# Kernel optimization log

Measured on AMD Instinct MI355X. Metric: run time of the kernel, lower is better.

## Reference

```python
import jax, jax.numpy as jnp
import numpy as np

B, S, DIM = 1, 2048, 1024
HEADS, KV_HEADS, DH = 16, 2, 64
GQ = HEADS // KV_HEADS
CBS = 64   # compress block size
SBS = 64   # selection block size
NUM_SEL = 8
WIN = 512  # sliding window size
NUM_MEM = 1
SCALE = DH ** -0.5
NEG = -jnp.finfo(jnp.float32).max


def setup_inputs():
    ks = jax.random.split(jax.random.key(0), 12)
    cdim = CBS * DH
    dim_inner = HEADS * DH
    dim_kv = KV_HEADS * DH
    p = lambda k, shape: jax.random.normal(k, shape, jnp.float32) * 0.02
    return {
        "x": jax.random.normal(ks[0], (B, S, DIM), jnp.float32),
        "rms_g": jnp.ones((DIM,), jnp.float32),
        "W_qkv": p(ks[1], (DIM, dim_inner + 2 * dim_kv)),
        "k_pos": p(ks[2], (KV_HEADS, CBS, DH)),
        "v_pos": p(ks[3], (KV_HEADS, CBS, DH)),
        "mem_kv": p(ks[4], (2, KV_HEADS, NUM_MEM, DH)),
        "kW1": p(ks[5], (cdim, cdim)), "kb1": jnp.zeros((cdim,), jnp.float32),
        "kW2": p(ks[6], (cdim, DH)), "kb2": jnp.zeros((DH,), jnp.float32),
        "vW1": p(ks[7], (cdim, cdim)), "vb1": jnp.zeros((cdim,), jnp.float32),
        "vW2": p(ks[8], (cdim, DH)), "vb2": jnp.zeros((DH,), jnp.float32),
        "W_comb": p(ks[9], (DIM, 3 * HEADS)),
        "b_comb": jnp.tile(jnp.array([-2.0, -2.0, 2.0], jnp.float32), HEADS),
        "W_out": p(ks[10], (HEADS * DH, DIM)),
    }


def _rot_half(u):
    v = u.reshape(u.shape[:-1] + (DH // 2, 2))
    return jnp.stack([-v[..., 1], v[..., 0]], axis=-1).reshape(u.shape)


def reference(x, rms_g, W_qkv, k_pos, v_pos, mem_kv, kW1, kb1, kW2, kb2,
              vW1, vb1, vW2, vb2, W_comb, b_comb, W_out):
    n_cb = S // CBS
    n_fb = S // SBS
    num_sel = min(NUM_SEL, n_cb)

    # RMSNorm
    xn = x * jax.lax.rsqrt(jnp.mean(x * x, -1, keepdims=True) + jnp.finfo(jnp.float32).eps) * rms_g

    qkv = xn @ W_qkv
    q, k, v = jnp.split(qkv, [HEADS * DH, (HEADS + KV_HEADS) * DH], axis=-1)
    q = q.reshape(B, S, HEADS, DH).transpose(0, 2, 1, 3)       # b h n d
    k = k.reshape(B, S, KV_HEADS, DH).transpose(0, 2, 1, 3)
    v = v.reshape(B, S, KV_HEADS, DH).transpose(0, 2, 1, 3)

    # ---- compressed branch: per-block MLP compression of K/V ----
    kc = (k + jnp.tile(k_pos, (1, n_cb, 1))[None]).reshape(B, KV_HEADS, n_cb, CBS * DH)
    vc = (v + jnp.tile(v_pos, (1, n_cb, 1))[None]).reshape(B, KV_HEADS, n_cb, CBS * DH)
    ck = jax.nn.relu(kc @ kW1 + kb1) @ kW2 + kb2               # b h w d
    cv = jax.nn.relu(vc @ vW1 + vb1) @ vW2 + vb2
    ck = jnp.concatenate([jnp.broadcast_to(mem_kv[0], (B, KV_HEADS, NUM_MEM, DH)), ck], axis=2)
    cv = jnp.concatenate([jnp.broadcast_to(mem_kv[1], (B, KV_HEADS, NUM_MEM, DH)), cv], axis=2)
    ck_seq = jnp.concatenate([jnp.full((NUM_MEM,), -1), (jnp.arange(n_cb) + 1) * CBS - 1])
    cmask = ck_seq[None, :] < jnp.arange(S)[:, None]           # [S, mem+n_cb]
    qg = q.reshape(B, KV_HEADS, GQ, S, DH)
    csim = jnp.einsum('bhgid,bhjd->bhgij', qg, ck) * SCALE
    csim = jnp.where(cmask, csim, NEG)
    c_out = jnp.einsum('bhgij,bhjd->bhgid', jax.nn.softmax(csim, -1), cv).reshape(B, HEADS, S, DH)

    # ---- rotary embedding (interleaved pairs, theta=10000) ----
    inv_freq = 1.0 / (10000.0 ** (jnp.arange(0, DH, 2, dtype=jnp.float32) / DH))
    freqs = jnp.repeat(jnp.arange(S, dtype=jnp.float32)[:, None] * inv_freq, 2, axis=-1)
    cos, sin = jnp.cos(freqs), jnp.sin(freqs)
    rq = q * cos + _rot_half(q) * sin
    rk = k * cos + _rot_half(k) * sin

    # ---- block selection from compressed attention scores ----
    imp = csim[..., NUM_MEM:].mean(axis=2)                     # mean over grouped queries: [B,KVH,S,n_cb]
    imp = jnp.concatenate([jnp.full(imp.shape[:-1] + (1,), -1000.0), imp], -1)
    imp = jax.nn.softmax(imp, -1)[..., 1:]
    sel_val, sel_idx = jax.lax.top_k(imp, num_sel)             # [B,KVH,S,sel]
    fmask = jnp.broadcast_to((sel_val > 1e-10)[..., None], (B, KV_HEADS, S, num_sel, SBS))
    diag_idx = jnp.broadcast_to((jnp.arange(S) // SBS)[None, None, :, None], (B, KV_HEADS, S, 1))
    sel_idx = jnp.concatenate([sel_idx, diag_idx], -1)         # append own (diagonal) block
    causal = jnp.tril(jnp.ones((SBS, SBS), bool))
    diag_mask = jnp.broadcast_to(jnp.tile(causal, (n_fb, 1))[None, None, :, None, :], (B, KV_HEADS, S, 1, SBS))
    fmask = jnp.concatenate([fmask, diag_mask], axis=-2).reshape(B, KV_HEADS, S, (num_sel + 1) * SBS)

    # ---- fine attention over gathered selected blocks ----
    fkb = rk.reshape(B, KV_HEADS, 1, n_fb, SBS, DH)
    fvb = v.reshape(B, KV_HEADS, 1, n_fb, SBS, DH)
    gi = sel_idx[..., None, None]                              # [B,KVH,S,sel+1,1,1]
    fk = jnp.take_along_axis(fkb, gi, axis=3).reshape(B, KV_HEADS, S, (num_sel + 1) * SBS, DH)
    fv = jnp.take_along_axis(fvb, gi, axis=3).reshape(B, KV_HEADS, S, (num_sel + 1) * SBS, DH)
    fqg = rq.reshape(B, KV_HEADS, GQ, S, DH)
    fsim = jnp.einsum('bhgid,bhijd->bhgij', fqg, fk) * SCALE
    fsim = jnp.where(fmask[:, :, None], fsim, NEG)
    f_out = jnp.einsum('bhgij,bhijd->bhgid', jax.nn.softmax(fsim, -1), fv).reshape(B, HEADS, S, DH)

    # ---- causal sliding window (exact window, look_backward=1) ----
    skf = jnp.repeat(rk, GQ, axis=1)
    svf = jnp.repeat(v, GQ, axis=1)
    nw = S // WIN
    kw = skf.reshape(B, HEADS, nw, WIN, DH)
    vw = svf.reshape(B, HEADS, nw, WIN, DH)
    kcat = jnp.concatenate([jnp.pad(kw, ((0, 0), (0, 0), (1, 0), (0, 0), (0, 0)))[:, :, :nw], kw], axis=3)
    vcat = jnp.concatenate([jnp.pad(vw, ((0, 0), (0, 0), (1, 0), (0, 0), (0, 0)))[:, :, :nw], vw], axis=3)
    qw = rq.reshape(B, HEADS, nw, WIN, DH)
    gq_pos = jnp.arange(nw)[:, None, None] * WIN + jnp.arange(WIN)[None, :, None]
    gk_pos = jnp.arange(nw)[:, None, None] * WIN - WIN + jnp.arange(2 * WIN)[None, None, :]
    smask = (gk_pos >= 0) & (gk_pos <= gq_pos) & (gq_pos - gk_pos <= WIN)
    ssim = jnp.where(smask, jnp.einsum('bhwid,bhwjd->bhwij', qw, kcat) * SCALE, NEG)
    s_out = jnp.einsum('bhwij,bhwjd->bhwid', jax.nn.softmax(ssim, -1), vcat).reshape(B, HEADS, S, DH)

    # ---- learned per-token, per-head strategy combination ----
    gates = jax.nn.sigmoid(xn @ W_comb + b_comb).reshape(B, S, HEADS, 3).transpose(0, 2, 1, 3)
    out = gates[..., 0:1] * c_out + gates[..., 1:2] * f_out + gates[..., 2:3] * s_out
    return out.transpose(0, 2, 1, 3).reshape(B, S, HEADS * DH) @ W_out
```

## Files before the change

kernel.cpp:

```cpp
#include <hip/hip_runtime.h>
#include <hip/hip_bf16.h>
#include <cstddef>
#include <cstdint>

#define S      2048
#define DIM    1024
#define HEADS  16
#define KVH    2
#define GQ     8
#define DH     64
#define CBS    64
#define SBS    64
#define NUMSEL 8
#define WIN    512
#define NCB    (S / CBS)
#define CDIM   (CBS * DH)
#define QKVC   (HEADS * DH + 2 * KVH * DH)
#define KOFF   (HEADS * DH)
#define VOFF   (HEADS * DH + KVH * DH)
#define SCALE  0.125f
#define RMS_EPS 1.1920928955078125e-07f

typedef __attribute__((ext_vector_type(8))) short bf16x8;
typedef __attribute__((ext_vector_type(4))) float f32x4;

__device__ inline short f2bs(float f) {
    __hip_bfloat16 b = __float2bfloat16(f);
    return *(short*)&b;
}

__device__ inline float wave_sum(float v) {
    for (int o = 32; o > 0; o >>= 1) v += __shfl_xor(v, o);
    return v;
}

__global__ __launch_bounds__(256) void rmsnorm_kernel(
        const float* __restrict__ x, const float* __restrict__ g,
        float* __restrict__ xn, __hip_bfloat16* __restrict__ xnb) {
    int s = blockIdx.x, tid = threadIdx.x;
    const float4* row = (const float4*)(x + (size_t)s * DIM);
    float4 v = row[tid];
    float ss = v.x * v.x + v.y * v.y + v.z * v.z + v.w * v.w;
    ss = wave_sum(ss);
    __shared__ float red[4];
    if ((tid & 63) == 0) red[tid >> 6] = ss;
    __syncthreads();
    float tot = red[0] + red[1] + red[2] + red[3];
    float sc = rsqrtf(tot / (float)DIM + RMS_EPS);
    float4 gg = ((const float4*)g)[tid];
    float4 o;
    o.x = v.x * sc * gg.x; o.y = v.y * sc * gg.y;
    o.z = v.z * sc * gg.z; o.w = v.w * sc * gg.w;
    ((float4*)(xn + (size_t)s * DIM))[tid] = o;
    size_t b = (size_t)s * DIM + tid * 4;
    xnb[b + 0] = __float2bfloat16(o.x);
    xnb[b + 1] = __float2bfloat16(o.y);
    xnb[b + 2] = __float2bfloat16(o.z);
    xnb[b + 3] = __float2bfloat16(o.w);
}

__global__ __launch_bounds__(256) void cast_bf16_kernel(
        const float* __restrict__ in, __hip_bfloat16* __restrict__ out, int n4) {
    int e = blockIdx.x * 256 + threadIdx.x;
    if (e >= n4) return;
    float4 v = ((const float4*)in)[e];
    out[4 * e + 0] = __float2bfloat16(v.x);
    out[4 * e + 1] = __float2bfloat16(v.y);
    out[4 * e + 2] = __float2bfloat16(v.z);
    out[4 * e + 3] = __float2bfloat16(v.w);
}

__global__ __launch_bounds__(256) void transpose_cast_kernel(
        const float* __restrict__ W, short* __restrict__ Wt, int K, int N) {
    __shared__ float tile[64][65];
    int n0 = blockIdx.x * 64, k0 = blockIdx.y * 64;
    int tid = threadIdx.x;
    #pragma unroll
    for (int e = 0; e < 16; e++) {
        int idx = tid + e * 256;
        int r = idx >> 6, c = idx & 63;
        float v = 0.f;
        if (n0 + c < N) v = W[(size_t)(k0 + r) * N + n0 + c];
        tile[r][c] = v;
    }
    __syncthreads();
    #pragma unroll
    for (int e = 0; e < 16; e++) {
        int idx = tid + e * 256;
        int r = idx >> 6, c = idx & 63;
        if (n0 + r < N)
            Wt[(size_t)(n0 + r) * K + k0 + c] = f2bs(tile[c][r]);
    }
}

__global__ __launch_bounds__(256) void cast_v_kernel(
        const float* __restrict__ qkv, short* __restrict__ vb) {
    int e = blockIdx.x * 256 + threadIdx.x;
    if (e >= S * KVH * DH / 4) return;
    int idx = e * 4;
    int tok = idx / (KVH * DH), rem = idx % (KVH * DH);
    float4 v = *(const float4*)(qkv + (size_t)tok * QKVC + VOFF + rem);
    vb[idx + 0] = f2bs(v.x);
    vb[idx + 1] = f2bs(v.y);
    vb[idx + 2] = f2bs(v.z);
    vb[idx + 3] = f2bs(v.w);
}

template <int BM, int BN, int WM, int WN, int ACT>
__global__ __launch_bounds__(256) void gemm_bt_kernel(
        const __hip_bfloat16* __restrict__ A, const short* __restrict__ Bt,
        const float* __restrict__ bias, float* __restrict__ C,
        int M, int N, int K) {
    constexpr int BK = 32;
    constexpr int TM = BM / (WM * 16);
    constexpr int TN = BN / (WN * 16);
    constexpr int LDK = BK + 8;
    __shared__ short As[BM][LDK];
    __shared__ short Bs[BN][LDK];
    int tid = threadIdx.x;
    int wave = tid >> 6, lane = tid & 63;
    int wm = wave % WM, wn = wave / WM;
    int m0 = wm * TM * 16, n0 = wn * TN * 16;
    int bm = blockIdx.y * BM, bn = blockIdx.x * BN;
    int lm = lane & 15, quad = lane >> 4;
    const short* Ash = (const short*)A;
    f32x4 acc[TM][TN] = {};
    for (int k0 = 0; k0 < K; k0 += BK) {
        #pragma unroll
        for (int e = 0; e < BM * BK / (256 * 8); e++) {
            int idx = (tid + e * 256) * 8;
            int r = idx >> 5, kk = idx & 31;
            *(bf16x8*)(&As[r][kk]) =
                *(const bf16x8*)(Ash + (size_t)(bm + r) * K + k0 + kk);
        }
        #pragma unroll
        for (int e = 0; e < BN * BK / (256 * 8); e++) {
            int idx = (tid + e * 256) * 8;
            int r = idx >> 5, kk = idx & 31;
            bf16x8 v = {};
            if (bn + r < N)
                v = *(const bf16x8*)(Bt + (size_t)(bn + r) * K + k0 + kk);
            *(bf16x8*)(&Bs[r][kk]) = v;
        }
        __syncthreads();
        bf16x8 af[TM], bf_[TN];
        #pragma unroll
        for (int i = 0; i < TM; i++)
            af[i] = *(const bf16x8*)(&As[m0 + i * 16 + lm][quad * 8]);
        #pragma unroll
        for (int j = 0; j < TN; j++)
            bf_[j] = *(const bf16x8*)(&Bs[n0 + j * 16 + lm][quad * 8]);
        #pragma unroll
        for (int i = 0; i < TM; i++)
            #pragma unroll
            for (int j = 0; j < TN; j++)
                acc[i][j] = __builtin_amdgcn_mfma_f32_16x16x32_bf16(
                    af[i], bf_[j], acc[i][j], 0, 0, 0);
        __syncthreads();
    }
    #pragma unroll
    for (int i = 0; i < TM; i++) {
        #pragma unroll
        for (int j = 0; j < TN; j++) {
            int gn = bn + n0 + j * 16 + lm;
            if (gn >= N) continue;
            #pragma unroll
            for (int r = 0; r < 4; r++) {
                int gm = bm + m0 + i * 16 + quad * 4 + r;
                float v = acc[i][j][r];
                if (bias) v += bias[gn];
                if (ACT == 2) v = 1.f / (1.f + expf(-v));
                C[(size_t)gm * N + gn] = v;
            }
        }
    }
}

template <int BM, int BN, int WM, int WN>
__global__ __launch_bounds__(256) void gemm_mfma_kernel(
        const __hip_bfloat16* __restrict__ A, const float* __restrict__ B,
        float* __restrict__ C, int M, int N, int K, int kslice) {
    constexpr int BK = 32;
    constexpr int TM = BM / (WM * 16);
    constexpr int TN = BN / (WN * 16);
    constexpr int LDK = BK + 8;
    constexpr int NB = BN * BK / 256;
    __shared__ __hip_bfloat16 As[BM][LDK];
    __shared__ __hip_bfloat16 Bs[BN][LDK];
    int tid = threadIdx.x;
    int wave = tid >> 6, lane = tid & 63;
    int wm = wave % WM, wn = wave / WM;
    int m0 = wm * TM * 16, n0 = wn * TN * 16;
    int bm = blockIdx.y * BM, bn = blockIdx.x * BN;
    int kbeg = blockIdx.z * kslice, kend = kbeg + kslice;
    int lm = lane & 15, quad = lane >> 4;
    f32x4 acc[TM][TN] = {};
    for (int k0 = kbeg; k0 < kend; k0 += BK) {
        #pragma unroll
        for (int e = 0; e < BM * BK / (256 * 8); e++) {
            int idx = (tid + e * 256) * 8;
            int r = idx >> 5, kk = idx & 31;
            *(bf16x8*)(&As[r][kk]) =
                *(const bf16x8*)(A + (size_t)(bm + r) * K + k0 + kk);
        }
        float tmpB[NB];
        #pragma unroll
        for (int e = 0; e < NB; e++) {
            int idx = tid + e * 256;
            int kk = idx / BN, n = idx % BN;
            tmpB[e] = B[(size_t)(k0 + kk) * N + bn + n];
        }
        #pragma unroll
        for (int e = 0; e < NB; e++) {
            int idx = tid + e * 256;
            int kk = idx / BN, n = idx % BN;
            Bs[n][kk] = __float2bfloat16(tmpB[e]);
        }
        __syncthreads();
        bf16x8 af[TM], bf_[TN];
        #pragma unroll
        for (int i = 0; i < TM; i++)
            af[i] = *(const bf16x8*)(&As[m0 + i * 16 + lm][quad * 8]);
        #pragma unroll
        for (int j = 0; j < TN; j++)
            bf_[j] = *(const bf16x8*)(&Bs[n0 + j * 16 + lm][quad * 8]);
        #pragma unroll
        for (int i = 0; i < TM; i++)
            #pragma unroll
            for (int j = 0; j < TN; j++)
                acc[i][j] = __builtin_amdgcn_mfma_f32_16x16x32_bf16(
                    af[i], bf_[j], acc[i][j], 0, 0, 0);
        __syncthreads();
    }
    size_t cbase = (size_t)blockIdx.z * M * N;
    #pragma unroll
    for (int i = 0; i < TM; i++) {
        #pragma unroll
        for (int j = 0; j < TN; j++) {
            int gn = bn + n0 + j * 16 + lm;
            #pragma unroll
            for (int r = 0; r < 4; r++) {
                int gm = bm + m0 + i * 16 + quad * 4 + r;
                C[cbase + (size_t)gm * N + gn] = acc[i][j][r];
            }
        }
    }
}

__global__ __launch_bounds__(256) void gemm_splitk_kernel(
        const float* __restrict__ A, const float* __restrict__ B,
        float* __restrict__ P, int M, int N, int K, int kslice) {
    const int BM = 64, BN = 64, BK = 16;
    __shared__ float As[BK][BM + 4];
    __shared__ float Bs[BK][BN];
    int bm = blockIdx.y * BM, bn = blockIdx.x * BN;
    int z = blockIdx.z;
    int kbeg = z * kslice, kend = kbeg + kslice;
    int tid = threadIdx.x;
    int tx = tid & 15, ty = tid >> 4;
    float acc[4][4] = {{0.f}};
    for (int k0 = kbeg; k0 < kend; k0 += BK) {
        #pragma unroll
        for (int e = 0; e < 4; e++) {
            int idx = tid + e * 256;
            int m = idx >> 4, kk = idx & 15;
            int gm = bm + m;
            As[kk][m] = (gm < M) ? A[(size_t)gm * K + k0 + kk] : 0.f;
        }
        #pragma unroll
        for (int e = 0; e < 4; e++) {
            int idx = tid + e * 256;
            int kk = idx >> 6, n = idx & 63;
            int gn = bn + n;
            Bs[kk][n] = (gn < N) ? B[(size_t)(k0 + kk) * N + gn] : 0.f;
        }
        __syncthreads();
        #pragma unroll
        for (int kk = 0; kk < BK; kk++) {
            float a[4], b[4];
            #pragma unroll
            for (int i = 0; i < 4; i++) a[i] = As[kk][ty * 4 + i];
            #pragma unroll
            for (int j = 0; j < 4; j++) b[j] = Bs[kk][tx * 4 + j];
            #pragma unroll
            for (int i = 0; i < 4; i++)
                #pragma unroll
                for (int j = 0; j < 4; j++) acc[i][j] += a[i] * b[j];
        }
        __syncthreads();
    }
    #pragma unroll
    for (int i = 0; i < 4; i++) {
        int gm = bm + ty * 4 + i;
        if (gm >= M) continue;
        #pragma unroll
        for (int j = 0; j < 4; j++) {
            int gn = bn + tx * 4 + j;
            if (gn >= N) continue;
            P[((size_t)z * M + gm) * N + gn] = acc[i][j];
        }
    }
}

template <int ACT>
__global__ __launch_bounds__(256) void reduce_splitk_kernel(
        const float* __restrict__ P, const float* __restrict__ bias,
        float* __restrict__ C, int MN, int N, int splits) {
    int e = blockIdx.x * 256 + threadIdx.x;
    if (e >= MN) return;
    float s = 0.f;
    for (int z = 0; z < splits; z++) s += P[(size_t)z * MN + e];
    s += bias[e % N];
    if (ACT == 1) s = fmaxf(s, 0.f);
    C[e] = s;
}

__global__ __launch_bounds__(256) void rotary_kernel(
        const float* __restrict__ qkv, short* __restrict__ rqb, short* __restrict__ rkb) {
    int s = blockIdx.x, tid = threadIdx.x;
    for (int p = tid; p < (HEADS + KVH) * (DH / 2); p += 256) {
        int t; const float* src; short* dst;
        if (p < HEADS * (DH / 2)) {
            int h = p >> 5; t = p & 31;
            src = qkv + (size_t)s * QKVC + h * DH + 2 * t;
            dst = rqb + (size_t)s * (HEADS * DH) + h * DH + 2 * t;
        } else {
            int pp = p - HEADS * (DH / 2);
            int h = pp >> 5; t = pp & 31;
            src = qkv + (size_t)s * QKVC + KOFF + h * DH + 2 * t;
            dst = rkb + (size_t)s * (KVH * DH) + h * DH + 2 * t;
        }
        float u0 = src[0], u1 = src[1];
        float freq = powf(10000.f, -((float)(2 * t) / (float)DH));
        float ang = (float)s * freq;
        float sn, cs;
        sincosf(ang, &sn, &cs);
        dst[0] = f2bs(u0 * cs - u1 * sn);
        dst[1] = f2bs(u1 * cs + u0 * sn);
    }
}

__global__ __launch_bounds__(256) void build_cmat_kernel(
        const float* __restrict__ qkv, const float* __restrict__ k_pos,
        const float* __restrict__ v_pos, __hip_bfloat16* __restrict__ kcm,
        __hip_bfloat16* __restrict__ vcm) {
    int r = blockIdx.x;
    int h = r >> 5, w = r & 31;
    for (int e = threadIdx.x; e < CDIM; e += 256) {
        int i = e >> 6, d = e & 63;
        size_t qb = (size_t)(w * CBS + i) * QKVC;
        kcm[(size_t)r * CDIM + e] =
            __float2bfloat16(qkv[qb + KOFF + h * DH + d] + k_pos[(h * CBS + i) * DH + d]);
        vcm[(size_t)r * CDIM + e] =
            __float2bfloat16(qkv[qb + VOFF + h * DH + d] + v_pos[(h * CBS + i) * DH + d]);
    }
}

__global__ __launch_bounds__(256) void assemble_kernel(
        const float* __restrict__ ckb, const float* __restrict__ cvb,
        const float* __restrict__ mem_kv, float* __restrict__ ck, float* __restrict__ cv,
        short* __restrict__ ck16, short* __restrict__ cv16) {
    int e = blockIdx.x * 256 + threadIdx.x;
    if (e >= KVH * (NCB + 1) * DH) return;
    int d = e & 63;
    int j = (e >> 6) % (NCB + 1);
    int h = e / ((NCB + 1) * DH);
    float kv, vv;
    if (j == 0) {
        kv = mem_kv[0 * KVH * DH + h * DH + d];
        vv = mem_kv[1 * KVH * DH + h * DH + d];
    } else {
        kv = ckb[((size_t)h * NCB + j - 1) * DH + d];
        vv = cvb[((size_t)h * NCB + j - 1) * DH + d];
    }
    ck[e] = kv; cv[e] = vv;
    ck16[e] = f2bs(kv); cv16[e] = f2bs(vv);
}

__global__ __launch_bounds__(64) void imp_kernel(
        const float* __restrict__ qkv, const float* __restrict__ ck,
        float* __restrict__ imp) {
    int kvh = blockIdx.x, s = blockIdx.y, t = threadIdx.x;
    __shared__ float qg[GQ * DH];
    __shared__ float ckl[NCB * 65];
    for (int e = t; e < GQ * DH; e += 64) {
        int g = e >> 6, d = e & 63;
        qg[e] = qkv[(size_t)s * QKVC + (kvh * GQ + g) * DH + d];
    }
    for (int e = t; e < NCB * DH; e += 64) {
        int w = e >> 6, d = e & 63;
        ckl[w * 65 + d] = ck[((size_t)kvh * (NCB + 1) + 1 + w) * DH + d];
    }
    __syncthreads();
    if (t < NCB) {
        int w = t;
        float val;
        if (w * CBS + CBS - 1 < s) {
            float acc = 0.f;
            #pragma unroll
            for (int g = 0; g < GQ; g++) {
                const float* qp = qg + g * DH;
                const float* cp = ckl + w * 65;
                #pragma unroll 16
                for (int d = 0; d < DH; d++) acc += qp[d] * cp[d];
            }
            val = acc * SCALE * (1.f / (float)GQ);
        } else {
            val = -INFINITY;
        }
        imp[((size_t)kvh * S + s) * NCB + w] = val;
    }
}

__global__ __launch_bounds__(256) void select_kernel(
        const float* __restrict__ imp, int* __restrict__ sel) {
    int idx = blockIdx.x * 256 + threadIdx.x;
    if (idx >= KVH * S) return;
    const float* row = imp + (size_t)idx * NCB;
    float p[NCB];
    float m = -1000.f;
    for (int w = 0; w < NCB; w++) { p[w] = row[w]; m = fmaxf(m, p[w]); }
    float z = expf(-1000.f - m);
    for (int w = 0; w < NCB; w++) { p[w] = expf(p[w] - m); z += p[w]; }
    float inv = 1.f / z;
    bool used[NCB];
    for (int w = 0; w < NCB; w++) used[w] = false;
    for (int i = 0; i < NUMSEL; i++) {
        int best = 0; float bv = -1.f;
        for (int w = 0; w < NCB; w++) {
            if (!used[w]) {
                float pw = p[w] * inv;
                if (pw > bv) { bv = pw; best = w; }
            }
        }
        used[best] = true;
        sel[(size_t)idx * NUMSEL + i] = (bv > 1e-10f) ? best : -1;
    }
}

__global__ __launch_bounds__(256) void cattn_kernel(
        const float* __restrict__ qkv, const short* __restrict__ ck16,
        const short* __restrict__ cv16, const float* __restrict__ gates,
        float* __restrict__ attn) {
    int h = blockIdx.x, qb = blockIdx.y;
    int kvh = h >> 3;
    int tid = threadIdx.x;
    int wv = tid >> 6, lane = tid & 63;
    int lm = lane & 15, quad = lane >> 4;
    __shared__ short Qb[64][72];
    __shared__ short Ks[64][72];
    __shared__ short Vt[64][72];
    __shared__ short Pb[64][72];
    for (int e = tid; e < 1024; e += 256) {
        int q = e >> 4, d4 = (e & 15) * 4;
        float4 v = *(const float4*)(qkv + (size_t)(qb * 64 + q) * QKVC + h * DH + d4);
        Qb[q][d4 + 0] = f2bs(v.x); Qb[q][d4 + 1] = f2bs(v.y);
        Qb[q][d4 + 2] = f2bs(v.z); Qb[q][d4 + 3] = f2bs(v.w);
    }
    for (int e = tid; e < 512; e += 256) {
        int c8 = e >> 6, j = e & 63;
        bf16x8 kv = {}, vv = {};
        if (j < NCB + 1) {
            kv = *(const bf16x8*)(ck16 + ((size_t)kvh * (NCB + 1) + j) * DH + c8 * 8);
            vv = *(const bf16x8*)(cv16 + ((size_t)kvh * (NCB + 1) + j) * DH + c8 * 8);
        }
        #pragma unroll
        for (int t = 0; t < 8; t++) {
            Ks[j][c8 * 8 + t] = kv[t];
            Vt[c8 * 8 + t][j] = vv[t];
        }
    }
    __syncthreads();
    bf16x8 aq0 = *(const bf16x8*)&Qb[wv * 16 + lm][quad * 8];
    bf16x8 aq1 = *(const bf16x8*)&Qb[wv * 16 + lm][32 + quad * 8];
    int vismax = (qb < NCB) ? qb : NCB;
    f32x4 sc[4];
    #pragma unroll
    for (int t = 0; t < 4; t++) {
        bf16x8 bk0 = *(const bf16x8*)&Ks[t * 16 + lm][quad * 8];
        bf16x8 bk1 = *(const bf16x8*)&Ks[t * 16 + lm][32 + quad * 8];
        f32x4 s4 = {0.f, 0.f, 0.f, 0.f};
        s4 = __builtin_amdgcn_mfma_f32_16x16x32_bf16(aq0, bk0, s4, 0, 0, 0);
        s4 = __builtin_amdgcn_mfma_f32_16x16x32_bf16(aq1, bk1, s4, 0, 0, 0);
        sc[t] = s4;
    }
    float l[4];
    float pr[4][4];
    #pragma unroll
    for (int r = 0; r < 4; r++) {
        float mx = -INFINITY;
        #pragma unroll
        for (int t = 0; t < 4; t++) {
            int jj = t * 16 + lm;
            bool vis = (jj == 0) || (jj <= vismax);
            float v = vis ? sc[t][r] * SCALE : -INFINITY;
            sc[t][r] = v;
            mx = fmaxf(mx, v);
        }
        #pragma unroll
        for (int o = 1; o < 16; o <<= 1) mx = fmaxf(mx, __shfl_xor(mx, o));
        float sum = 0.f;
        #pragma unroll
        for (int t = 0; t < 4; t++) {
            float p = expf(sc[t][r] - mx);
            pr[r][t] = p;
            sum += p;
        }
        #pragma unroll
        for (int o = 1; o < 16; o <<= 1) sum += __shfl_xor(sum, o);
        l[r] = sum;
    }
    #pragma unroll
    for (int r = 0; r < 4; r++)
        #pragma unroll
        for (int t = 0; t < 4; t++)
            Pb[wv * 16 + quad * 4 + r][t * 16 + lm] = f2bs(pr[r][t]);
    __syncthreads();
    bf16x8 ap0 = *(const bf16x8*)&Pb[wv * 16 + lm][quad * 8];
    bf16x8 ap1 = *(const bf16x8*)&Pb[wv * 16 + lm][32 + quad * 8];
    f32x4 oacc[4];
    #pragma unroll
    for (int t = 0; t < 4; t++) {
        bf16x8 bv0 = *(const bf16x8*)&Vt[t * 16 + lm][quad * 8];
        bf16x8 bv1 = *(const bf16x8*)&Vt[t * 16 + lm][32 + quad * 8];
        f32x4 a = {0.f, 0.f, 0.f, 0.f};
        a = __builtin_amdgcn_mfma_f32_16x16x32_bf16(ap0, bv0, a, 0, 0, 0);
        a = __builtin_amdgcn_mfma_f32_16x16x32_bf16(ap1, bv1, a, 0, 0, 0);
        oacc[t] = a;
    }
    #pragma unroll
    for (int r = 0; r < 4; r++) {
        int spos = qb * 64 + wv * 16 + quad * 4 + r;
        float g0 = gates[((size_t)spos * HEADS + h) * 3 + 0];
        float f = g0 / l[r];
        #pragma unroll
        for (int t = 0; t < 4; t++)
            attn[(size_t)spos * (HEADS * DH) + h * DH + t * 16 + lm] = oacc[t][r] * f;
    }
}

__global__ __launch_bounds__(256) void fattn_kernel(
        const short* __restrict__ rqb, const short* __restrict__ rkb,
        const short* __restrict__ vb, const int* __restrict__ sel,
        const float* __restrict__ gates, float* __restrict__ attn) {
    int kvh = blockIdx.x, s = blockIdx.y;
    int tid = threadIdx.x;
    int wv = tid >> 6, lane = tid & 63;
    int lm = lane & 15, quad = lane >> 4;
    int hh = tid >> 5, lk = tid & 31;
    __shared__ short Qb[16][68];
    __shared__ short Vt[64][68];
    __shared__ short Pb[16][68];
    __shared__ float Sc[8][68];
    __shared__ float alph[8], fac[8];
    __shared__ int bl[9];
    for (int e = tid; e < 512; e += 256) {
        int h = e >> 6, d = e & 63;
        Qb[h][d] = rqb[(size_t)s * (HEADS * DH) + (kvh * 8 + h) * DH + d];
    }
    if (tid < NUMSEL) bl[tid] = sel[((size_t)kvh * S + s) * NUMSEL + tid];
    if (tid == NUMSEL) bl[NUMSEL] = s >> 6;
    __syncthreads();
    bf16x8 aq0 = *(const bf16x8*)&Qb[lm][quad * 8];
    bf16x8 aq1 = *(const bf16x8*)&Qb[lm][32 + quad * 8];
    float mh = -INFINITY, lh = 0.f;
    f32x4 oacc = {0.f, 0.f, 0.f, 0.f};
    for (int i = 0; i < 9; i++) {
        int w = bl[i];
        if (i < NUMSEL && w < 0) continue;
        #pragma unroll
        for (int r = 0; r < 2; r++) {
            int idx = tid + r * 256;
            int c8 = idx >> 6, j = idx & 63;
            bf16x8 vv = *(const bf16x8*)(vb + ((size_t)(w * SBS + j) * KVH + kvh) * DH + c8 * 8);
            #pragma unroll
            for (int t = 0; t < 8; t++) Vt[c8 * 8 + t][j] = vv[t];
        }
        {
            const short* kp = rkb + ((size_t)(w * SBS + wv * 16 + lm) * KVH + kvh) * DH;
            bf16x8 bk0 = *(const bf16x8*)(kp + quad * 8);
            bf16x8 bk1 = *(const bf16x8*)(kp + 32 + quad * 8);
            f32x4 sc4 = {0.f, 0.f, 0.f, 0.f};
            sc4 = __builtin_amdgcn_mfma_f32_16x16x32_bf16(aq0, bk0, sc4, 0, 0, 0);
            sc4 = __builtin_amdgcn_mfma_f32_16x16x32_bf16(aq1, bk1, sc4, 0, 0, 0);
            bool vis = (i < NUMSEL) || (wv * 16 + lm <= (s & 63));
            #pragma unroll
            for (int r = 0; r < 4; r++) {
                int row = quad * 4 + r;
                if (row < 8) Sc[row][wv * 16 + lm] = vis ? sc4[r] * SCALE : -INFINITY;
            }
        }
        __syncthreads();
        {
            float s0 = Sc[hh][lk], s1 = Sc[hh][lk + 32];
            float bmx = fmaxf(s0, s1);
            #pragma unroll
            for (int o = 1; o < 32; o <<= 1) bmx = fmaxf(bmx, __shfl_xor(bmx, o));
            float mn = fmaxf(mh, bmx);
            float scl = expf(mh - mn);
            float p0 = expf(s0 - mn), p1 = expf(s1 - mn);
            float rs = p0 + p1;
            #pragma unroll
            for (int o = 1; o < 32; o <<= 1) rs += __shfl_xor(rs, o);
            lh = lh * scl + rs;
            mh = mn;
            Pb[hh][lk] = f2bs(p0);
            Pb[hh][lk + 32] = f2bs(p1);
            if (lk == 0) alph[hh] = scl;
        }
        __syncthreads();
        {
            bf16x8 ap0 = *(const bf16x8*)&Pb[lm][quad * 8];
            bf16x8 ap1 = *(const bf16x8*)&Pb[lm][32 + quad * 8];
            bf16x8 bv0 = *(const bf16x8*)&Vt[wv * 16 + lm][quad * 8];
            bf16x8 bv1 = *(const bf16x8*)&Vt[wv * 16 + lm][32 + quad * 8];
            #pragma unroll
            for (int r = 0; r < 4; r++) oacc[r] *= alph[(quad * 4 + r) & 7];
            oacc = __builtin_amdgcn_mfma_f32_16x16x32_bf16(ap0, bv0, oacc, 0, 0, 0);
            oacc = __builtin_amdgcn_mfma_f32_16x16x32_bf16(ap1, bv1, oacc, 0, 0, 0);
        }
        __syncthreads();
    }
    if (lk == 0)
        fac[hh] = gates[((size_t)s * HEADS + kvh * 8 + hh) * 3 + 1] / lh;
    __syncthreads();
    #pragma unroll
    for (int r = 0; r < 4; r++) {
        int row = quad * 4 + r;
        if (row < 8)
            attn[(size_t)s * (HEADS * DH) + (kvh * 8 + row) * DH + wv * 16 + lm]
                += oacc[r] * fac[row];
    }
}

__global__ __launch_bounds__(256) void sattn_kernel(
        const short* __restrict__ rqb, const short* __restrict__ rkb,
        const short* __restrict__ vb, const float* __restrict__ gates,
        float* __restrict__ attn) {
    int h = blockIdx.x, qb = blockIdx.y;
    int kvh = h >> 3;
    int tid = threadIdx.x;
    int wv = tid >> 6, lane = tid & 63;
    int lm = lane & 15, quad = lane >> 4;
    __shared__ short Vt[64][72];
    __shared__ short Pb[64][72];
    const short* qp = rqb + (size_t)(qb * 64 + wv * 16 + lm) * (HEADS * DH) + h * DH;
    bf16x8 aq0 = *(const bf16x8*)(qp + quad * 8);
    bf16x8 aq1 = *(const bf16x8*)(qp + 32 + quad * 8);
    int myrow = wv * 16 + quad * 4;
    float m[4], l[4];
    f32x4 oacc[4];
    #pragma unroll
    for (int r = 0; r < 4; r++) { m[r] = -INFINITY; l[r] = 0.f; }
    #pragma unroll
    for (int t = 0; t < 4; t++) oacc[t] = (f32x4){0.f, 0.f, 0.f, 0.f};
    for (int c = 0; c < 9; c++) {
        int kb = qb * 64 - WIN + c * 64;
        if (kb < 0) continue;
        for (int e = tid; e < 512; e += 256) {
            int c8 = e >> 6, j = e & 63;
            bf16x8 vv = *(const bf16x8*)(vb + ((size_t)(kb + j) * KVH + kvh) * DH + c8 * 8);
            #pragma unroll
            for (int t = 0; t < 8; t++) Vt[c8 * 8 + t][j] = vv[t];
        }
        f32x4 sc[4];
        #pragma unroll
        for (int t = 0; t < 4; t++) {
            const short* kp = rkb + ((size_t)(kb + t * 16 + lm) * KVH + kvh) * DH;
            bf16x8 bk0 = *(const bf16x8*)(kp + quad * 8);
            bf16x8 bk1 = *(const bf16x8*)(kp + 32 + quad * 8);
            f32x4 s4 = {0.f, 0.f, 0.f, 0.f};
            s4 = __builtin_amdgcn_mfma_f32_16x16x32_bf16(aq0, bk0, s4, 0, 0, 0);
            s4 = __builtin_amdgcn_mfma_f32_16x16x32_bf16(aq1, bk1, s4, 0, 0, 0);
            sc[t] = s4;
        }
        float pr[4][4];
        #pragma unroll
        for (int r = 0; r < 4; r++) {
            int row = myrow + r;
            float mx = -INFINITY;
            #pragma unroll
            for (int t = 0; t < 4; t++) {
                int jj = t * 16 + lm;
                bool vis = true;
                if (c == 0) vis = (jj >= row);
                if (c == 8) vis = (jj <= row);
                float v = vis ? sc[t][r] * SCALE : -INFINITY;
                sc[t][r] = v;
                mx = fmaxf(mx, v);
            }
            #pragma unroll
            for (int o = 1; o < 16; o <<= 1) mx = fmaxf(mx, __shfl_xor(mx, o));
            float mn = fmaxf(m[r], mx);
            float al = expf(m[r] - mn);
            float sum = 0.f;
            #pragma unroll
            for (int t = 0; t < 4; t++) {
                float p = expf(sc[t][r] - mn);
                pr[r][t] = p;
                sum += p;
            }
            #pragma unroll
            for (int o = 1; o < 16; o <<= 1) sum += __shfl_xor(sum, o);
            l[r] = l[r] * al + sum;
            m[r] = mn;
            #pragma unroll
            for (int t = 0; t < 4; t++) oacc[t][r] *= al;
        }
        __syncthreads();
        #pragma unroll
        for (int r = 0; r < 4; r++)
            #pragma unroll
            for (int t = 0; t < 4; t++)
                Pb[myrow + r][t * 16 + lm] = f2bs(pr[r][t]);
        __syncthreads();
        bf16x8 ap0 = *(const bf16x8*)&Pb[wv * 16 + lm][quad * 8];
        bf16x8 ap1 = *(const bf16x8*)&Pb[wv * 16 + lm][32 + quad * 8];
        #pragma unroll
        for (int t = 0; t < 4; t++) {
            bf16x8 bv0 = *(const bf16x8*)&Vt[t * 16 + lm][quad * 8];
            bf16x8 bv1 = *(const bf16x8*)&Vt[t * 16 + lm][32 + quad * 8];
            oacc[t] = __builtin_amdgcn_mfma_f32_16x16x32_bf16(ap0, bv0, oacc[t], 0, 0, 0);
            oacc[t] = __builtin_amdgcn_mfma_f32_16x16x32_bf16(ap1, bv1, oacc[t], 0, 0, 0);
        }
        __syncthreads();
    }
    #pragma unroll
    for (int r = 0; r < 4; r++) {
        int spos = qb * 64 + myrow + r;
        float g2 = gates[((size_t)spos * HEADS + h) * 3 + 2];
        float f = g2 / l[r];
        #pragma unroll
        for (int t = 0; t < 4; t++)
            attn[(size_t)spos * (HEADS * DH) + h * DH + t * 16 + lm] += oacc[t][r] * f;
    }
}

extern "C" void kernel_launch(void* const* d_in, const int* in_sizes, int n_in,
                              void* d_out, int out_size, void* d_ws, size_t ws_size,
                              hipStream_t stream) {
    const float* x      = (const float*)d_in[0];
    const float* rms_g  = (const float*)d_in[1];
    const float* W_qkv  = (const float*)d_in[2];
    const float* k_pos  = (const float*)d_in[3];
    const float* v_pos  = (const float*)d_in[4];
    const float* mem_kv = (const float*)d_in[5];
    const float* kW1    = (const float*)d_in[6];
    const float* kb1    = (const float*)d_in[7];
    const float* kW2    = (const float*)d_in[8];
    const float* kb2    = (const float*)d_in[9];
    const float* vW1    = (const float*)d_in[10];
    const float* vb1    = (const float*)d_in[11];
    const float* vW2    = (const float*)d_in[12];
    const float* vb2    = (const float*)d_in[13];
    const float* W_comb = (const float*)d_in[14];
    const float* b_comb = (const float*)d_in[15];
    const float* W_out  = (const float*)d_in[16];
    float* out = (float*)d_out;

    float* ws    = (float*)d_ws;
    float* xn    = ws;
    float* qkv   = xn    + (size_t)S * DIM;
    short* rqb   = (short*)(qkv + (size_t)S * QKVC);
    short* rkb   = (short*)((float*)rqb + 1048576);
    float* R     = (float*)rkb + 131072;
    float* ck    = R     + 1048576;
    float* cv    = ck    + (size_t)KVH * (NCB + 1) * DH;
    short* ck16  = (short*)(cv + (size_t)KVH * (NCB + 1) * DH);
    short* cv16  = (short*)((float*)ck16 + 2112);
    float* imp   = (float*)cv16 + 2112;
    float* gates = imp   + (size_t)KVH * S * NCB;
    float* attn  = gates + (size_t)S * HEADS * 3;
    int*   sel   = (int*)(attn + (size_t)S * HEADS * DH);
    float* WT    = attn + (size_t)S * HEADS * DH + 8192;
    short* wqkvT = (short*)WT;
    short* woutT = (short*)(WT + 655360);
    short* wcombT= (short*)(WT + 655360 + 524288);

    __hip_bfloat16* xnb   = (__hip_bfloat16*)R;
    __hip_bfloat16* kcmb  = (__hip_bfloat16*)R;
    __hip_bfloat16* vcmb  = (__hip_bfloat16*)(R + 131072);
    float* khid  = R + 262144;
    float* vhid  = R + 524288;
    float* ckb   = R + 786432;
    float* cvb   = R + 790528;
    __hip_bfloat16* attnb = (__hip_bfloat16*)R;
    short* vbb   = (short*)imp;
    float* partW1 = attn;
    float* partW2 = imp;

    transpose_cast_kernel<<<dim3(QKVC / 64, DIM / 64), 256, 0, stream>>>(W_qkv, wqkvT, DIM, QKVC);
    transpose_cast_kernel<<<dim3(DIM / 64, DIM / 64), 256, 0, stream>>>(W_out, woutT, DIM, DIM);
    transpose_cast_kernel<<<dim3(1, DIM / 64), 256, 0, stream>>>(W_comb, wcombT, DIM, HEADS * 3);
    rmsnorm_kernel<<<S, 256, 0, stream>>>(x, rms_g, xn, xnb);
    gemm_bt_kernel<64, 64, 2, 2, 0><<<dim3(QKVC / 64, S / 64), 256, 0, stream>>>(
        xnb, wqkvT, nullptr, qkv, S, QKVC, DIM);
    gemm_bt_kernel<64, 64, 2, 2, 2><<<dim3(1, S / 64), 256, 0, stream>>>(
        xnb, wcombT, b_comb, gates, S, HEADS * 3, DIM);
    rotary_kernel<<<S, 256, 0, stream>>>(qkv, rqb, rkb);
    build_cmat_kernel<<<KVH * NCB, 256, 0, stream>>>(qkv, k_pos, v_pos, kcmb, vcmb);
    gemm_mfma_kernel<64, 128, 1, 4><<<dim3(CDIM / 128, 1, 8), 256, 0, stream>>>(
        kcmb, kW1, partW1, 64, CDIM, CDIM, CDIM / 8);
    reduce_splitk_kernel<1><<<(64 * CDIM + 255) / 256, 256, 0, stream>>>(
        partW1, kb1, khid, 64 * CDIM, CDIM, 8);
    gemm_splitk_kernel<<<dim3(1, 1, 32), 256, 0, stream>>>(khid, kW2, partW2, 64, DH, CDIM, CDIM / 32);
    reduce_splitk_kernel<0><<<(64 * DH + 255) / 256, 256, 0, stream>>>(partW2, kb2, ckb, 64 * DH, DH, 32);
    gemm_mfma_kernel<64, 128, 1, 4><<<dim3(CDIM / 128, 1, 8), 256, 0, stream>>>(
        vcmb, vW1, partW1, 64, CDIM, CDIM, CDIM / 8);
    reduce_splitk_kernel<1><<<(64 * CDIM + 255) / 256, 256, 0, stream>>>(
        partW1, vb1, vhid, 64 * CDIM, CDIM, 8);
    gemm_splitk_kernel<<<dim3(1, 1, 32), 256, 0, stream>>>(vhid, vW2, partW2, 64, DH, CDIM, CDIM / 32);
    reduce_splitk_kernel<0><<<(64 * DH + 255) / 256, 256, 0, stream>>>(partW2, vb2, cvb, 64 * DH, DH, 32);
    assemble_kernel<<<(KVH * (NCB + 1) * DH + 255) / 256, 256, 0, stream>>>(
        ckb, cvb, mem_kv, ck, cv, ck16, cv16);
    imp_kernel<<<dim3(KVH, S), 64, 0, stream>>>(qkv, ck, imp);
    select_kernel<<<(KVH * S + 255) / 256, 256, 0, stream>>>(imp, sel);
    cast_v_kernel<<<(S * KVH * DH / 4 + 255) / 256, 256, 0, stream>>>(qkv, vbb);
    cattn_kernel<<<dim3(HEADS, S / 64), 256, 0, stream>>>(qkv, ck16, cv16, gates, attn);
    fattn_kernel<<<dim3(KVH, S), 256, 0, stream>>>(rqb, rkb, vbb, sel, gates, attn);
    sattn_kernel<<<dim3(HEADS, S / 64), 256, 0, stream>>>(rqb, rkb, vbb, gates, attn);
    cast_bf16_kernel<<<(S * HEADS * DH / 4 + 255) / 256, 256, 0, stream>>>(
        attn, attnb, S * HEADS * DH / 4);
    gemm_bt_kernel<64, 64, 2, 2, 0><<<dim3(DIM / 64, S / 64), 256, 0, stream>>>(
        attnb, woutT, nullptr, out, S, DIM, DIM);
}
```

Measured before the change: 553.9 us.

## Rewrite fine-attention kernel as single-wave block with register softmax

The selected-block attention kernel now runs one 64-lane wave per (kv head, query) instead of four waves. Scores, online softmax and the output accumulators stay in registers, and the max and sum reductions use 16-lane shuffles. This removes the shared-memory score buffer and the three block barriers per selected block. In exchange each wave does four times the MFMA and V-transpose work serially, and it relies on an lgkmcnt wait instead of a barrier for the P exchange.

```diff
diff --git a/kernel.cpp b/kernel.cpp
--- a/kernel.cpp
+++ b/kernel.cpp
@@ -539,97 +539,112 @@
     }
 }
 
-__global__ __launch_bounds__(256) void fattn_kernel(
+__global__ __launch_bounds__(64, 4) void fattn_kernel(
         const short* __restrict__ rqb, const short* __restrict__ rkb,
         const short* __restrict__ vb, const int* __restrict__ sel,
         const float* __restrict__ gates, float* __restrict__ attn) {
     int kvh = blockIdx.x, s = blockIdx.y;
-    int tid = threadIdx.x;
-    int wv = tid >> 6, lane = tid & 63;
+    int lane = threadIdx.x;
     int lm = lane & 15, quad = lane >> 4;
-    int hh = tid >> 5, lk = tid & 31;
-    __shared__ short Qb[16][68];
     __shared__ short Vt[64][68];
     __shared__ short Pb[16][68];
-    __shared__ float Sc[8][68];
-    __shared__ float alph[8], fac[8];
-    __shared__ int bl[9];
-    for (int e = tid; e < 512; e += 256) {
-        int h = e >> 6, d = e & 63;
-        Qb[h][d] = rqb[(size_t)s * (HEADS * DH) + (kvh * 8 + h) * DH + d];
-    }
-    if (tid < NUMSEL) bl[tid] = sel[((size_t)kvh * S + s) * NUMSEL + tid];
-    if (tid == NUMSEL) bl[NUMSEL] = s >> 6;
-    __syncthreads();
-    bf16x8 aq0 = *(const bf16x8*)&Qb[lm][quad * 8];
-    bf16x8 aq1 = *(const bf16x8*)&Qb[lm][32 + quad * 8];
-    float mh = -INFINITY, lh = 0.f;
-    f32x4 oacc = {0.f, 0.f, 0.f, 0.f};
+    const short* qp = rqb + (size_t)s * (HEADS * DH) + (size_t)(kvh * 8 + (lm & 7)) * DH;
+    bf16x8 aq0 = *(const bf16x8*)(qp + quad * 8);
+    bf16x8 aq1 = *(const bf16x8*)(qp + 32 + quad * 8);
+    int bl[9];
+    {
+        const int4* sp = (const int4*)(sel + ((size_t)kvh * S + s) * NUMSEL);
+        int4 s0 = sp[0], s1 = sp[1];
+        bl[0] = s0.x; bl[1] = s0.y; bl[2] = s0.z; bl[3] = s0.w;
+        bl[4] = s1.x; bl[5] = s1.y; bl[6] = s1.z; bl[7] = s1.w;
+        bl[8] = s >> 6;
+    }
+    float m[4], l[4];
+    f32x4 oacc[4];
+    #pragma unroll
+    for (int r = 0; r < 4; r++) {
+        m[r] = -INFINITY; l[r] = 0.f;
+        oacc[r] = (f32x4){0.f, 0.f, 0.f, 0.f};
+    }
     for (int i = 0; i < 9; i++) {
         int w = bl[i];
         if (i < NUMSEL && w < 0) continue;
-        #pragma unroll
-        for (int r = 0; r < 2; r++) {
-            int idx = tid + r * 256;
-            int c8 = idx >> 6, j = idx & 63;
-            bf16x8 vv = *(const bf16x8*)(vb + ((size_t)(w * SBS + j) * KVH + kvh) * DH + c8 * 8);
-            #pragma unroll
-            for (int t = 0; t < 8; t++) Vt[c8 * 8 + t][j] = vv[t];
-        }
-        {
-            const short* kp = rkb + ((size_t)(w * SBS + wv * 16 + lm) * KVH + kvh) * DH;
+        const short* vp = vb + ((size_t)(w * SBS + lane) * KVH + kvh) * DH;
+        bf16x8 vv[8];
+        #pragma unroll
+        for (int r = 0; r < 8; r++) vv[r] = *(const bf16x8*)(vp + r * 8);
+        f32x4 sc[4];
+        #pragma unroll
+        for (int t = 0; t < 4; t++) {
+            const short* kp = rkb + ((size_t)(w * SBS + t * 16 + lm) * KVH + kvh) * DH;
             bf16x8 bk0 = *(const bf16x8*)(kp + quad * 8);
             bf16x8 bk1 = *(const bf16x8*)(kp + 32 + quad * 8);
-            f32x4 sc4 = {0.f, 0.f, 0.f, 0.f};
-            sc4 = __builtin_amdgcn_mfma_f32_16x16x32_bf16(aq0, bk0, sc4, 0, 0, 0);
-            sc4 = __builtin_amdgcn_mfma_f32_16x16x32_bf16(aq1, bk1, sc4, 0, 0, 0);
-            bool vis = (i < NUMSEL) || (wv * 16 + lm <= (s & 63));
-            #pragma unroll
-            for (int r = 0; r < 4; r++) {
-                int row = quad * 4 + r;
-                if (row < 8) Sc[row][wv * 16 + lm] = vis ? sc4[r] * SCALE : -INFINITY;
+            f32x4 s4 = {0.f, 0.f, 0.f, 0.f};
+            s4 = __builtin_amdgcn_mfma_f32_16x16x32_bf16(aq0, bk0, s4, 0, 0, 0);
+            s4 = __builtin_amdgcn_mfma_f32_16x16x32_bf16(aq1, bk1, s4, 0, 0, 0);
+            sc[t] = s4;
+        }
+        #pragma unroll
+        for (int r = 0; r < 8; r++)
+            #pragma unroll
+            for (int t = 0; t < 8; t++) Vt[r * 8 + t][lane] = vv[r][t];
+        float pr[4][4];
+        bool diag = (i == NUMSEL);
+        #pragma unroll
+        for (int r = 0; r < 4; r++) {
+            float mx = -INFINITY;
+            #pragma unroll
+            for (int t = 0; t < 4; t++) {
+                int jj = t * 16 + lm;
+                bool vis = !diag || (jj <= (s & 63));
+                float v = vis ? sc[t][r] * SCALE : -INFINITY;
+                sc[t][r] = v;
+                mx = fmaxf(mx, v);
             }
-        }
-        __syncthreads();
-        {
-            float s0 = Sc[hh][lk], s1 = Sc[hh][lk + 32];
-            float bmx = fmaxf(s0, s1);
-            #pragma unroll
-            for (int o = 1; o < 32; o <<= 1) bmx = fmaxf(bmx, __shfl_xor(bmx, o));
-            float mn = fmaxf(mh, bmx);
-            float scl = expf(mh - mn);
-            float p0 = expf(s0 - mn), p1 = expf(s1 - mn);
-            float rs = p0 + p1;
-            #pragma unroll
-            for (int o = 1; o < 32; o <<= 1) rs += __shfl_xor(rs, o);
-            lh = lh * scl + rs;
-            mh = mn;
-            Pb[hh][lk] = f2bs(p0);
-            Pb[hh][lk + 32] = f2bs(p1);
-            if (lk == 0) alph[hh] = scl;
-        }
-        __syncthreads();
-        {
-            bf16x8 ap0 = *(const bf16x8*)&Pb[lm][quad * 8];
-            bf16x8 ap1 = *(const bf16x8*)&Pb[lm][32 + quad * 8];
-            bf16x8 bv0 = *(const bf16x8*)&Vt[wv * 16 + lm][quad * 8];
-            bf16x8 bv1 = *(const bf16x8*)&Vt[wv * 16 + lm][32 + quad * 8];
-            #pragma unroll
-            for (int r = 0; r < 4; r++) oacc[r] *= alph[(quad * 4 + r) & 7];
-            oacc = __builtin_amdgcn_mfma_f32_16x16x32_bf16(ap0, bv0, oacc, 0, 0, 0);
-            oacc = __builtin_amdgcn_mfma_f32_16x16x32_bf16(ap1, bv1, oacc, 0, 0, 0);
-        }
-        __syncthreads();
-    }
-    if (lk == 0)
-        fac[hh] = gates[((size_t)s * HEADS + kvh * 8 + hh) * 3 + 1] / lh;
-    __syncthreads();
-    #pragma unroll
-    for (int r = 0; r < 4; r++) {
-        int row = quad * 4 + r;
-        if (row < 8)
-            attn[(size_t)s * (HEADS * DH) + (kvh * 8 + row) * DH + wv * 16 + lm]
-                += oacc[r] * fac[row];
+            #pragma unroll
+            for (int o = 1; o < 16; o <<= 1) mx = fmaxf(mx, __shfl_xor(mx, o));
+            float mn = fmaxf(m[r], mx);
+            float al = __expf(m[r] - mn);
+            float sum = 0.f;
+            #pragma unroll
+            for (int t = 0; t < 4; t++) {
+                float p = __expf(sc[t][r] - mn);
+                pr[r][t] = p;
+                sum += p;
+            }
+            #pragma unroll
+            for (int o = 1; o < 16; o <<= 1) sum += __shfl_xor(sum, o);
+            l[r] = l[r] * al + sum;
+            m[r] = mn;
+            #pragma unroll
+            for (int t = 0; t < 4; t++) oacc[t][r] *= al;
+        }
+        #pragma unroll
+        for (int r = 0; r < 4; r++)
+            #pragma unroll
+            for (int t = 0; t < 4; t++)
+                Pb[quad * 4 + r][t * 16 + lm] = f2bs(pr[r][t]);
+        asm volatile("s_waitcnt lgkmcnt(0)" ::: "memory");
+        bf16x8 ap0 = *(const bf16x8*)&Pb[lm][quad * 8];
+        bf16x8 ap1 = *(const bf16x8*)&Pb[lm][32 + quad * 8];
+        #pragma unroll
+        for (int t = 0; t < 4; t++) {
+            bf16x8 bv0 = *(const bf16x8*)&Vt[t * 16 + lm][quad * 8];
+            bf16x8 bv1 = *(const bf16x8*)&Vt[t * 16 + lm][32 + quad * 8];
+            oacc[t] = __builtin_amdgcn_mfma_f32_16x16x32_bf16(ap0, bv0, oacc[t], 0, 0, 0);
+            oacc[t] = __builtin_amdgcn_mfma_f32_16x16x32_bf16(ap1, bv1, oacc[t], 0, 0, 0);
+        }
+    }
+    if (quad < 2) {
+        #pragma unroll
+        for (int r = 0; r < 4; r++) {
+            int head = kvh * 8 + quad * 4 + r;
+            float fac = gates[((size_t)s * HEADS + head) * 3 + 1] / l[r];
+            #pragma unroll
+            for (int t = 0; t < 4; t++)
+                attn[(size_t)s * (HEADS * DH) + head * DH + t * 16 + lm]
+                    += oacc[t][r] * fac;
+        }
     }
 }
 
@@ -817,7 +832,7 @@
     select_kernel<<<(KVH * S + 255) / 256, 256, 0, stream>>>(imp, sel);
     cast_v_kernel<<<(S * KVH * DH / 4 + 255) / 256, 256, 0, stream>>>(qkv, vbb);
     cattn_kernel<<<dim3(HEADS, S / 64), 256, 0, stream>>>(qkv, ck16, cv16, gates, attn);
-    fattn_kernel<<<dim3(KVH, S), 256, 0, stream>>>(rqb, rkb, vbb, sel, gates, attn);
+    fattn_kernel<<<dim3(KVH, S), 64, 0, stream>>>(rqb, rkb, vbb, sel, gates, attn);
     sattn_kernel<<<dim3(HEADS, S / 64), 256, 0, stream>>>(rqb, rkb, vbb, gates, attn);
     cast_bf16_kernel<<<(S * HEADS * DH / 4 + 255) / 256, 256, 0, stream>>>(
         attn, attnb, S * HEADS * DH / 4);
```

New measurement: 547.2 us. Within noise of the previous version (-1.2%).
